# Kernel tuning notes

Measured on AMD Instinct MI355X. Metric: run time of the kernel, lower is better.

The kernel has to match this reference:

```python
import jax, jax.numpy as jnp
import numpy as np

SUBDIV = 5      # icosphere subdivision level -> V = 10*4^5 + 2 = 10242
BATCH = 8
C_IN = 128
C_OUT = 128


def build_icosphere(n_sub):
    t = (1.0 + 5.0 ** 0.5) / 2.0
    verts = [np.array(v, dtype=np.float64) for v in [
        (-1, t, 0), (1, t, 0), (-1, -t, 0), (1, -t, 0),
        (0, -1, t), (0, 1, t), (0, -1, -t), (0, 1, -t),
        (t, 0, -1), (t, 0, 1), (-t, 0, -1), (-t, 0, 1)]]
    verts = [v / np.linalg.norm(v) for v in verts]
    faces = [(0, 11, 5), (0, 5, 1), (0, 1, 7), (0, 7, 10), (0, 10, 11),
             (1, 5, 9), (5, 11, 4), (11, 10, 2), (10, 7, 6), (7, 1, 8),
             (3, 9, 4), (3, 4, 2), (3, 2, 6), (3, 6, 8), (3, 8, 9),
             (4, 9, 5), (2, 4, 11), (6, 2, 10), (8, 6, 7), (9, 8, 1)]
    cache = {}

    def midpoint(a, b):
        key = (min(a, b), max(a, b))
        if key in cache:
            return cache[key]
        m = verts[a] + verts[b]
        m = m / np.linalg.norm(m)
        verts.append(m)
        cache[key] = len(verts) - 1
        return cache[key]

    for _ in range(n_sub):
        new_faces = []
        for a, b, c in faces:
            ab, bc, ca = midpoint(a, b), midpoint(b, c), midpoint(c, a)
            new_faces += [(a, ab, ca), (b, bc, ab), (c, ca, bc), (ab, bc, ca)]
        faces = new_faces
    edges = set()
    for a, b, c in faces:
        for u, v in ((a, b), (b, c), (c, a)):
            edges.add((min(u, v), max(u, v)))
    return np.stack(verts), sorted(edges)


def get_neighbors(nbr_vert, edges):
    nb = [[] for _ in range(nbr_vert)]
    for v1, v2 in edges:
        nb[v1].append(v2)
        nb[v2].append(v1)
    return nb


def sort_neighbors(nb):
    # walk the 1-ring so consecutive neighbors share an edge (same as torch code)
    out = []
    for i in range(len(nb)):
        rem = nb[i].copy()
        v = rem[0]
        s = [v]
        rem.remove(v)
        while rem:
            common = list(set(rem).intersection(nb[v]))
            v = common[0]
            s.append(v)
            rem.remove(v)
        out.append(s)
    return out


def sort_rotation(verts, nb):
    # orient the ring consistently (faithful to torch version incl. the >1 test)
    out = []
    for i, s in enumerate(nb):
        p0, p1, p2 = verts[i], verts[s[0]], verts[s[1]]
        v1 = p1 - p0
        v2 = p2 - p1
        vn = np.cross(v1, v2)
        n = vn / np.linalg.norm(vn)
        cg = p0 + 2.0 * ((p1 + v2 / 2.0) - p0) / 3.0
        out.append(list(s) if float(np.dot(n, cg)) > 1.0 else list(reversed(s)))
    return out


def build_patch_index():
    verts, edges = build_icosphere(SUBDIV)
    nb = sort_rotation(verts, sort_neighbors(get_neighbors(len(verts), edges)))
    V = len(verts)
    idx = np.zeros((V, 9), dtype=np.int32)
    mask = np.zeros((V, 9), dtype=np.float32)
    for i, ring in enumerate(nb):
        idx[i, 0] = i          # mat[i][i*9] = 1 -> self at slot 0
        mask[i, 0] = 1.0
        for j, v in enumerate(ring):  # neighbor j at slot j+1
            idx[i, j + 1] = v
            mask[i, j + 1] = 1.0
    return idx, mask


def setup_inputs() -> dict:
    idx, mask = build_patch_index()
    V = idx.shape[0]
    key = jax.random.key(0)
    k1, k2, k3 = jax.random.split(key, 3)
    x = jax.random.normal(k1, (BATCH, V, C_IN), dtype=jnp.float32)
    w = jax.random.normal(k2, (C_OUT, C_IN, 3, 3), dtype=jnp.float32) / np.sqrt(C_IN * 9.0)
    b = jax.random.normal(k3, (C_OUT,), dtype=jnp.float32) * 0.01
    return {"x": x, "w": w, "b": b,
            "nbr_idx": jnp.asarray(idx), "nbr_mask": jnp.asarray(mask)}


def reference(x, w, b, nbr_idx, nbr_mask):
    # x: [B, V, C]. The torch mm with the one-hot mat_neighbors is exactly a
    # gather of (self + up-to-6 ring neighbors) into a 3x3 patch, zero-padded.
    patches = x[:, nbr_idx, :] * nbr_mask[None, :, :, None]   # [B, V, 9, C]
    wk = w.reshape(C_OUT, C_IN, 9)                            # 3x3 kernel, valid conv on 3x3 patch
    out = jnp.einsum('bvkc,ock->bvo', patches, wk) + b        # [B, V, C_OUT]
    return out
```

## Files before the change

### kernel.cpp

```cpp
#include <hip/hip_runtime.h>
#include <hip/hip_bf16.h>


#define V_CNT    10242
#define CC       128
#define KS_ACT   7
#define BM       64
#define VT_PER_B 161
#define BATCH    8

typedef short short8 __attribute__((ext_vector_type(8)));
typedef float f32x4  __attribute__((ext_vector_type(4)));

__device__ __forceinline__ unsigned f2bf(float f) {
    unsigned u = __float_as_uint(f);
    u += 0x7fffu + ((u >> 16) & 1u);
    return u >> 16;
}

#define XB_OFF 0
#define WB_OFF 20975616
#define ZP_OFF 21204992

#define XB_BLOCKS 5121
#define WB_BLOCKS 448

__global__ void prep_kernel(const float* __restrict__ x, const float* __restrict__ w,
                            unsigned short* __restrict__ xb, unsigned short* __restrict__ wb,
                            unsigned short* __restrict__ zp, int n8) {
    int b = blockIdx.x;
    if (b < XB_BLOCKS) {
        int i = b * 256 + threadIdx.x;
        if (i < n8) {
            const float4* s = (const float4*)(x + (size_t)i * 8);
            float4 a = s[0], c = s[1];
            uint4 p;
            p.x = f2bf(a.x) | (f2bf(a.y) << 16);
            p.y = f2bf(a.z) | (f2bf(a.w) << 16);
            p.z = f2bf(c.x) | (f2bf(c.y) << 16);
            p.w = f2bf(c.z) | (f2bf(c.w) << 16);
            *(uint4*)(xb + (size_t)i * 8) = p;
        }
    } else if (b < XB_BLOCKS + WB_BLOCKS) {
        int i = (b - XB_BLOCKS) * 256 + threadIdx.x;
        int k = i >> 14;
        int r = i & 16383;
        int o = r >> 7;
        int c = r & 127;
        wb[i] = (unsigned short)f2bf(w[(o * CC + c) * 9 + k]);
    } else {
        if (threadIdx.x < 128) zp[threadIdx.x] = 0;
    }
}

__global__ __launch_bounds__(256, 4)
void icoconv_kernel(const unsigned short* __restrict__ xb,
                    const unsigned short* __restrict__ wb,
                    const unsigned short* __restrict__ zp,
                    const float* __restrict__ bias,
                    const int* __restrict__ nidx,
                    const float* __restrict__ nmask,
                    float* __restrict__ out) {
    __shared__ __align__(16) char smem[64 * 132 * 4];
    unsigned short* As0 = (unsigned short*)smem;
    unsigned short* As1 = (unsigned short*)(smem + 16384);
    float* Os = (float*)smem;

    const int tid  = threadIdx.x;
    const int lane = tid & 63;
    const int wid  = tid >> 6;
    const int bb   = blockIdx.x & 7;
    const int vt   = blockIdx.x >> 3;
    const int vbase = vt * BM;

    const int sr = tid >> 2;
    const int sh = tid & 3;
    const int v  = vbase + sr;
    const bool valid = v < V_CNT;

    int gidx[KS_ACT];
    unsigned mbits = 0;
    #pragma unroll
    for (int k = 0; k < KS_ACT; ++k) {
        int g = 0; float mk = 0.f;
        if (valid) { g = nidx[v * 9 + k]; mk = nmask[v * 9 + k]; }
        gidx[k] = g;
        mbits |= (mk != 0.f ? 1u : 0u) << k;
    }
    const unsigned short* xbatch = xb + (size_t)bb * V_CNT * CC;

    f32x4 acc[4][2];
    #pragma unroll
    for (int i = 0; i < 4; ++i)
        #pragma unroll
        for (int j = 0; j < 2; ++j)
            acc[i][j] = f32x4{0.f, 0.f, 0.f, 0.f};

    const unsigned short* wlane = wb + (wid * 32 + (lane & 15)) * CC + ((lane >> 4) << 3);

    const int swz  = (sr & 7) << 4;
    const int hi16 = (lane >> 4) << 4;

    uint4 pf[4];
    {
        const unsigned short* s = ((mbits & 1u) ? (xbatch + (size_t)gidx[0] * CC) : zp) + sh * 32;
        #pragma unroll
        for (int q = 0; q < 4; ++q) pf[q] = *(const uint4*)(s + q * 8);
    }
    {
        char* wdst = (char*)As0 + sr * 256;
        #pragma unroll
        for (int q = 0; q < 4; ++q)
            *(uint4*)(wdst + ((sh * 64 + q * 16) ^ swz)) = pf[q];
    }
    {
        const unsigned short* s = (((mbits >> 1) & 1u) ? (xbatch + (size_t)gidx[1] * CC) : zp) + sh * 32;
        #pragma unroll
        for (int q = 0; q < 4; ++q) pf[q] = *(const uint4*)(s + q * 8);
    }
    __syncthreads();

    #pragma unroll
    for (int t = 0; t < KS_ACT; ++t) {
        const unsigned short* bcur = (t & 1) ? As1 : As0;
        unsigned short*       bnxt = (t & 1) ? As0 : As1;

        if (t < KS_ACT - 1) {
            char* wdst = (char*)bnxt + sr * 256;
            #pragma unroll
            for (int q = 0; q < 4; ++q)
                *(uint4*)(wdst + ((sh * 64 + q * 16) ^ swz)) = pf[q];
        }

        const unsigned short* wks = wlane + t * (CC * CC);
        short8 bfr[4][2];
        #pragma unroll
        for (int kk = 0; kk < 4; ++kk)
            #pragma unroll
            for (int ni = 0; ni < 2; ++ni)
                bfr[kk][ni] = *(const short8*)(wks + ni * 16 * CC + kk * 32);

        if (t < KS_ACT - 2) {
            const int k2 = t + 2;
            const unsigned short* s =
                (((mbits >> k2) & 1u) ? (xbatch + (size_t)gidx[k2] * CC) : zp) + sh * 32;
            #pragma unroll
            for (int q = 0; q < 4; ++q) pf[q] = *(const uint4*)(s + q * 8);
        }

        #pragma unroll
        for (int kk = 0; kk < 4; ++kk) {
            short8 af[4];
            #pragma unroll
            for (int mi = 0; mi < 4; ++mi) {
                int row = mi * 16 + (lane & 15);
                af[mi] = *(const short8*)((const char*)bcur + row * 256 +
                          ((kk * 64 + hi16) ^ ((row & 7) << 4)));
            }
            #pragma unroll
            for (int mi = 0; mi < 4; ++mi)
                #pragma unroll
                for (int ni = 0; ni < 2; ++ni)
                    acc[mi][ni] = __builtin_amdgcn_mfma_f32_16x16x32_bf16(af[mi], bfr[kk][ni], acc[mi][ni], 0, 0, 0);
        }

        if (t < KS_ACT - 1) __syncthreads();
    }

    __syncthreads();
    #pragma unroll
    for (int mi = 0; mi < 4; ++mi) {
        int lrow = mi * 16 + ((lane >> 4) << 2);
        #pragma unroll
        for (int ni = 0; ni < 2; ++ni) {
            int lcol = wid * 32 + ni * 16 + (lane & 15);
            #pragma unroll
            for (int j = 0; j < 4; ++j)
                Os[(lrow + j) * 132 + lcol] = acc[mi][ni][j];
        }
    }
    __syncthreads();

    {
        const int r  = tid >> 2;
        const int cb = (tid & 3) << 5;
        const int vv = vbase + r;
        if (vv < V_CNT) {
            float* op = out + ((size_t)bb * V_CNT + vv) * CC + cb;
            #pragma unroll
            for (int q = 0; q < 8; ++q) {
                f32x4 val = *(const f32x4*)(Os + r * 132 + cb + q * 4);
                f32x4 bv  = *(const f32x4*)(bias + cb + q * 4);
                val = val + bv;
                __builtin_nontemporal_store(val, (f32x4*)(op + q * 4));
            }
        }
    }
}

extern "C" void kernel_launch(void* const* d_in, const int* in_sizes, int n_in,
                              void* d_out, int out_size, void* d_ws, size_t ws_size,
                              hipStream_t stream) {
    const float* x     = (const float*)d_in[0];
    const float* w     = (const float*)d_in[1];
    const float* bias  = (const float*)d_in[2];
    const int*   nidx  = (const int*)d_in[3];
    const float* nmask = (const float*)d_in[4];
    float* out = (float*)d_out;

    unsigned short* xb = (unsigned short*)((char*)d_ws + XB_OFF);
    unsigned short* wb = (unsigned short*)((char*)d_ws + WB_OFF);
    unsigned short* zp = (unsigned short*)((char*)d_ws + ZP_OFF);

    int n8 = BATCH * V_CNT * CC / 8;
    prep_kernel<<<XB_BLOCKS + WB_BLOCKS + 1, 256, 0, stream>>>(x, w, xb, wb, zp, n8);

    icoconv_kernel<<<BATCH * VT_PER_B, 256, 0, stream>>>(xb, wb, zp, bias, nidx, nmask, out);
}
```

Baseline: 197.1 us.

## Load gathered MFMA A-fragments directly from global, drop LDS staging

Each lane now precomputes byte offsets for all of its rows and neighbor slots, pointing into the bf16 activation buffer or a zero pad. It reads the A-operand fragments straight from global memory instead of staging them through double-buffered shared memory. This removes the LDS write/read traffic and the per-tap barriers. In exchange each of the four waves reloads the same activation rows, so global/L2 traffic roughly quadruples, and 28 offset registers push occupancy down to 3 waves per SIMD. The zero pad is enlarged to cover the wider per-lane read range.

```diff
diff --git a/kernel.cpp b/kernel.cpp
--- a/kernel.cpp
+++ b/kernel.cpp
@@ -49,22 +49,18 @@
         int c = r & 127;
         wb[i] = (unsigned short)f2bf(w[(o * CC + c) * 9 + k]);
     } else {
-        if (threadIdx.x < 128) zp[threadIdx.x] = 0;
+        if (threadIdx.x < 256) zp[threadIdx.x] = 0;
     }
 }
 
-__global__ __launch_bounds__(256, 4)
-void icoconv_kernel(const unsigned short* __restrict__ xb,
+__global__ __launch_bounds__(256, 3)
+void icoconv_kernel(const char* __restrict__ wsb,
                     const unsigned short* __restrict__ wb,
-                    const unsigned short* __restrict__ zp,
                     const float* __restrict__ bias,
                     const int* __restrict__ nidx,
                     const float* __restrict__ nmask,
                     float* __restrict__ out) {
-    __shared__ __align__(16) char smem[64 * 132 * 4];
-    unsigned short* As0 = (unsigned short*)smem;
-    unsigned short* As1 = (unsigned short*)(smem + 16384);
-    float* Os = (float*)smem;
+    __shared__ __align__(16) float Os[64 * 132];
 
     const int tid  = threadIdx.x;
     const int lane = tid & 63;
@@ -73,21 +69,23 @@
     const int vt   = blockIdx.x >> 3;
     const int vbase = vt * BM;
 
-    const int sr = tid >> 2;
-    const int sh = tid & 3;
-    const int v  = vbase + sr;
-    const bool valid = v < V_CNT;
+    const int l15 = lane & 15;
+    const int khi = (lane >> 4) << 4;
 
-    int gidx[KS_ACT];
-    unsigned mbits = 0;
+    const int bbV = bb * V_CNT;
+    unsigned off[4][KS_ACT];
     #pragma unroll
-    for (int k = 0; k < KS_ACT; ++k) {
-        int g = 0; float mk = 0.f;
-        if (valid) { g = nidx[v * 9 + k]; mk = nmask[v * 9 + k]; }
-        gidx[k] = g;
-        mbits |= (mk != 0.f ? 1u : 0u) << k;
+    for (int mi = 0; mi < 4; ++mi) {
+        int r = vbase + mi * 16 + l15;
+        bool vv = r < V_CNT;
+        #pragma unroll
+        for (int k = 0; k < KS_ACT; ++k) {
+            int g = 0; float mk = 0.f;
+            if (vv) { g = nidx[r * 9 + k]; mk = nmask[r * 9 + k]; }
+            unsigned o = (mk != 0.f) ? (unsigned)((bbV + g) * 256) : (unsigned)ZP_OFF;
+            off[mi][k] = o + khi;
+        }
     }
-    const unsigned short* xbatch = xb + (size_t)bb * V_CNT * CC;
 
     f32x4 acc[4][2];
     #pragma unroll
@@ -96,42 +94,10 @@
         for (int j = 0; j < 2; ++j)
             acc[i][j] = f32x4{0.f, 0.f, 0.f, 0.f};
 
-    const unsigned short* wlane = wb + (wid * 32 + (lane & 15)) * CC + ((lane >> 4) << 3);
-
-    const int swz  = (sr & 7) << 4;
-    const int hi16 = (lane >> 4) << 4;
-
-    uint4 pf[4];
-    {
-        const unsigned short* s = ((mbits & 1u) ? (xbatch + (size_t)gidx[0] * CC) : zp) + sh * 32;
-        #pragma unroll
-        for (int q = 0; q < 4; ++q) pf[q] = *(const uint4*)(s + q * 8);
-    }
-    {
-        char* wdst = (char*)As0 + sr * 256;
-        #pragma unroll
-        for (int q = 0; q < 4; ++q)
-            *(uint4*)(wdst + ((sh * 64 + q * 16) ^ swz)) = pf[q];
-    }
-    {
-        const unsigned short* s = (((mbits >> 1) & 1u) ? (xbatch + (size_t)gidx[1] * CC) : zp) + sh * 32;
-        #pragma unroll
-        for (int q = 0; q < 4; ++q) pf[q] = *(const uint4*)(s + q * 8);
-    }
-    __syncthreads();
+    const unsigned short* wlane = wb + (wid * 32 + l15) * CC + (khi >> 1);
 
     #pragma unroll
     for (int t = 0; t < KS_ACT; ++t) {
-        const unsigned short* bcur = (t & 1) ? As1 : As0;
-        unsigned short*       bnxt = (t & 1) ? As0 : As1;
-
-        if (t < KS_ACT - 1) {
-            char* wdst = (char*)bnxt + sr * 256;
-            #pragma unroll
-            for (int q = 0; q < 4; ++q)
-                *(uint4*)(wdst + ((sh * 64 + q * 16) ^ swz)) = pf[q];
-        }
-
         const unsigned short* wks = wlane + t * (CC * CC);
         short8 bfr[4][2];
         #pragma unroll
@@ -140,40 +106,26 @@
             for (int ni = 0; ni < 2; ++ni)
                 bfr[kk][ni] = *(const short8*)(wks + ni * 16 * CC + kk * 32);
 
-        if (t < KS_ACT - 2) {
-            const int k2 = t + 2;
-            const unsigned short* s =
-                (((mbits >> k2) & 1u) ? (xbatch + (size_t)gidx[k2] * CC) : zp) + sh * 32;
-            #pragma unroll
-            for (int q = 0; q < 4; ++q) pf[q] = *(const uint4*)(s + q * 8);
-        }
-
         #pragma unroll
         for (int kk = 0; kk < 4; ++kk) {
             short8 af[4];
             #pragma unroll
-            for (int mi = 0; mi < 4; ++mi) {
-                int row = mi * 16 + (lane & 15);
-                af[mi] = *(const short8*)((const char*)bcur + row * 256 +
-                          ((kk * 64 + hi16) ^ ((row & 7) << 4)));
-            }
+            for (int mi = 0; mi < 4; ++mi)
+                af[mi] = *(const short8*)(wsb + off[mi][t] + kk * 64);
             #pragma unroll
             for (int mi = 0; mi < 4; ++mi)
                 #pragma unroll
                 for (int ni = 0; ni < 2; ++ni)
                     acc[mi][ni] = __builtin_amdgcn_mfma_f32_16x16x32_bf16(af[mi], bfr[kk][ni], acc[mi][ni], 0, 0, 0);
         }
-
-        if (t < KS_ACT - 1) __syncthreads();
     }
 
-    __syncthreads();
     #pragma unroll
     for (int mi = 0; mi < 4; ++mi) {
         int lrow = mi * 16 + ((lane >> 4) << 2);
         #pragma unroll
         for (int ni = 0; ni < 2; ++ni) {
-            int lcol = wid * 32 + ni * 16 + (lane & 15);
+            int lcol = wid * 32 + ni * 16 + l15;
             #pragma unroll
             for (int j = 0; j < 4; ++j)
                 Os[(lrow + j) * 132 + lcol] = acc[mi][ni][j];
@@ -215,5 +167,5 @@
     int n8 = BATCH * V_CNT * CC / 8;
     prep_kernel<<<XB_BLOCKS + WB_BLOCKS + 1, 256, 0, stream>>>(x, w, xb, wb, zp, n8);
 
-    icoconv_kernel<<<BATCH * VT_PER_B, 256, 0, stream>>>(xb, wb, zp, bias, nidx, nmask, out);
+    icoconv_kernel<<<BATCH * VT_PER_B, 256, 0, stream>>>((const char*)d_ws, wb, bias, nidx, nmask, out);
 }
```

Measured after the change: 261.9 us. 32.9% more time.
